# Performance work log

Hardware: AMD Instinct MI355X
Metric: run time of the kernel (lower is better)

## Reference

```python
import jax, jax.numpy as jnp
import numpy as np

B, P, E, C = 64, 10000, 128, 100


def setup_inputs() -> dict:
    key = jax.random.key(0)
    k1, k2, k3, k4 = jax.random.split(key, 4)
    encoded_nodes = jax.random.normal(k1, (B, P, E), dtype=jnp.float32)
    cluster_ids = jax.random.randint(k2, (B, P), 0, C, dtype=jnp.int64)
    # nn.Linear(E, E) params
    lim = 1.0 / np.sqrt(E)
    proj_w = jax.random.uniform(k3, (E, E), dtype=jnp.float32, minval=-lim, maxval=lim)
    proj_b = jax.random.uniform(k4, (E,), dtype=jnp.float32, minval=-lim, maxval=lim)
    return {"encoded_nodes": encoded_nodes, "cluster_ids": cluster_ids,
            "num_clusters": C, "proj_w": proj_w, "proj_b": proj_b}


def reference(encoded_nodes, cluster_ids, num_clusters, proj_w, proj_b):
    ids = cluster_ids.astype(jnp.int32)  # [B, P]

    def seg_sum(x, i):
        return jax.ops.segment_sum(x, i, num_segments=num_clusters)

    # per-batch scatter-add of node embeddings and counts
    sums = jax.vmap(seg_sum)(encoded_nodes, ids)                     # [B, C, E]
    ones = jnp.ones(encoded_nodes.shape[:2], encoded_nodes.dtype)    # [B, P]
    counts = jax.vmap(seg_sum)(ones, ids)[..., None]                  # [B, C, 1]

    cluster_embs = sums / jnp.maximum(counts, 1.0)                    # mean pooling
    cluster_embs = cluster_embs @ proj_w.T + proj_b                   # Linear(E, E)

    # gather each node's (projected) cluster embedding back
    idx = jnp.broadcast_to(ids[:, :, None], encoded_nodes.shape)      # [B, P, E]
    g_node = jnp.take_along_axis(cluster_embs, idx, axis=1)           # [B, P, E]
    return cluster_embs, g_node
```

## Files before the change

### kernel.cpp

```cpp
#include <hip/hip_runtime.h>

#define BB 64
#define PP 10000
#define EE 128
#define CC 100
#define NP 16
#define CHUNK (PP / NP)
#define ROWS (CC * EE)
#define PLANE (CC * 32)

typedef float v4f __attribute__((ext_vector_type(4)));

__global__ __launch_bounds__(256) void scatter_kernel(
    const float* __restrict__ nodes, const int* __restrict__ ids,
    float* __restrict__ psums, float* __restrict__ pcnts)
{
    __shared__ float s_acc[ROWS];
    __shared__ float s_cnt[CC];
    __shared__ int   s_ids[CHUNK];

    const int tid = threadIdx.x;
    const int b   = blockIdx.x;
    const int np  = blockIdx.y;

    for (int i = tid; i < ROWS; i += 256) s_acc[i] = 0.f;
    if (tid < CC) s_cnt[tid] = 0.f;

    const int p0 = np * CHUNK;
    const int* idb = ids + b * PP + p0;
    for (int i = tid; i < CHUNK; i += 256) s_ids[i] = idb[i];
    __syncthreads();

    const int lane = tid & 31;
    const int sub  = tid >> 5;
    const v4f* src = (const v4f*)(nodes + (size_t)b * PP * EE
                                        + (size_t)p0 * EE);

#pragma unroll 4
    for (int p = sub; p < CHUNK; p += 8) {
        int c = s_ids[p];
        v4f v = src[(size_t)p * 32 + lane];
        if ((unsigned)c < CC) {
            float* a = &s_acc[c * 32 + lane];
            __hip_atomic_fetch_add(a + 0 * PLANE, v.x, __ATOMIC_RELAXED, __HIP_MEMORY_SCOPE_WORKGROUP);
            __hip_atomic_fetch_add(a + 1 * PLANE, v.y, __ATOMIC_RELAXED, __HIP_MEMORY_SCOPE_WORKGROUP);
            __hip_atomic_fetch_add(a + 2 * PLANE, v.z, __ATOMIC_RELAXED, __HIP_MEMORY_SCOPE_WORKGROUP);
            __hip_atomic_fetch_add(a + 3 * PLANE, v.w, __ATOMIC_RELAXED, __HIP_MEMORY_SCOPE_WORKGROUP);
            if (lane == 0)
                __hip_atomic_fetch_add(&s_cnt[c], 1.0f, __ATOMIC_RELAXED, __HIP_MEMORY_SCOPE_WORKGROUP);
        }
    }
    __syncthreads();

    v4f* outp = (v4f*)(psums + (size_t)(np * BB + b) * ROWS);
    const v4f* accp = (const v4f*)s_acc;
    for (int i = tid; i < ROWS / 4; i += 256)
        __builtin_nontemporal_store(accp[i], &outp[i]);
    float* oc = pcnts + (np * BB + b) * CC;
    if (tid < CC) __builtin_nontemporal_store(s_cnt[tid], &oc[tid]);
}

__global__ __launch_bounds__(256) void project_kernel(
    float* __restrict__ ce,
    const float* __restrict__ psums,
    const float* __restrict__ pcnts,
    const float* __restrict__ W,
    const float* __restrict__ bias)
{
    __shared__ float s_wt[EE * 129];
    __shared__ float s_mt[EE * 8];
    __shared__ float s_inv[8];

    const int tid = threadIdx.x;
    for (int i = tid; i < EE * EE; i += 256) {
        int e = i >> 7, k = i & 127;
        s_wt[k * 129 + e] = W[i];
    }

    const int e   = tid & 127;
    const int sub = tid >> 7;
    const float be = bias[e];
    const int row0 = blockIdx.x * 16;

    for (int j = 0; j < 2; ++j) {
        __syncthreads();
        if (tid < 8) {
            int row = row0 + j * 8 + tid;
            float s = 0.f;
#pragma unroll
            for (int np = 0; np < NP; ++np)
                s += pcnts[np * (BB * CC) + row];
            s_inv[tid] = 1.0f / fmaxf(s, 1.0f);
        }
        for (int i = tid; i < 8 * EE; i += 256) {
            int rr = i >> 7, idx = i & 127;
            int row = row0 + j * 8 + rr;
            int bb = row / CC, c = row % CC;
            const float* pp = psums + (size_t)bb * ROWS
                                    + (idx >> 5) * PLANE + c * 32 + (idx & 31);
            float s = 0.f;
#pragma unroll
            for (int np = 0; np < NP; ++np)
                s += __builtin_nontemporal_load(pp + (size_t)np * BB * ROWS);
            int ee = ((idx & 31) << 2) | (idx >> 5);
            s_mt[ee * 8 + rr] = s;
        }
        __syncthreads();

        float acc0 = 0.f, acc1 = 0.f, acc2 = 0.f, acc3 = 0.f;
        const float* wp = &s_wt[e];
        const v4f* mp = (const v4f*)s_mt;
#pragma unroll 8
        for (int k = 0; k < 128; ++k) {
            float w = wp[k * 129];
            v4f   m = mp[k * 2 + sub];
            acc0 = fmaf(w, m.x, acc0);
            acc1 = fmaf(w, m.y, acc1);
            acc2 = fmaf(w, m.z, acc2);
            acc3 = fmaf(w, m.w, acc3);
        }
        const int rbase = row0 + j * 8 + sub * 4;
        ce[(size_t)(rbase + 0) * EE + e] = be + acc0 * s_inv[sub * 4 + 0];
        ce[(size_t)(rbase + 1) * EE + e] = be + acc1 * s_inv[sub * 4 + 1];
        ce[(size_t)(rbase + 2) * EE + e] = be + acc2 * s_inv[sub * 4 + 2];
        ce[(size_t)(rbase + 3) * EE + e] = be + acc3 * s_inv[sub * 4 + 3];
    }
}

__global__ __launch_bounds__(256) void gather_kernel(
    const int* __restrict__ ids, const float* __restrict__ ce,
    float* __restrict__ gn)
{
    const int tid  = threadIdx.x;
    const int lane = tid & 31;
    const int sub  = tid >> 5;
    const int b    = blockIdx.y;

    const int* idb = ids + b * PP;
    const v4f* ceb = (const v4f*)(ce + (size_t)b * CC * EE);
    v4f* dst = (v4f*)(gn + (size_t)b * PP * EE);

#pragma unroll 2
    for (int p = blockIdx.x * 8 + sub; p < PP; p += 32 * 8) {
        int c = idb[p];
        if ((unsigned)c >= CC) c = 0;
        v4f v = ceb[(size_t)c * 32 + lane];
        __builtin_nontemporal_store(v, &dst[(size_t)p * 32 + lane]);
    }
}

extern "C" void kernel_launch(void* const* d_in, const int* in_sizes, int n_in,
                              void* d_out, int out_size, void* d_ws, size_t ws_size,
                              hipStream_t stream)
{
    const float* nodes = (const float*)d_in[0];
    const int*   ids   = (const int*)d_in[1];
    const float* W     = (const float*)d_in[3];
    const float* bias  = (const float*)d_in[4];

    float* out = (float*)d_out;
    float* ce  = out;
    float* gn  = out + (size_t)BB * CC * EE;

    float* psums = gn;
    float* pcnts = gn + (size_t)NP * BB * ROWS;

    hipLaunchKernelGGL(scatter_kernel, dim3(BB, NP), dim3(256), 0, stream,
                       nodes, ids, psums, pcnts);
    hipLaunchKernelGGL(project_kernel, dim3(BB * CC / 16), dim3(256), 0, stream,
                       ce, psums, pcnts, W, bias);
    hipLaunchKernelGGL(gather_kernel, dim3(32, BB), dim3(256), 0, stream,
                       ids, ce, gn);
}
```

Before: 886.7 us.

## Fuse scatter and projection into one per-batch kernel without partial sums

Scatter-sum and the linear projection now run in a single kernel with one block per batch. Each block accumulates the whole point range in shared memory, normalises by the counts and projects in place, so the 16-way partial-sum buffers and their reduction pass are gone. In exchange only 64 blocks run on a GPU with far more compute units, so each block walks all 10000 points serially and the scatter phase loses most of its parallelism. W is now read from global memory per thread instead of a transposed shared-memory copy.

```diff
diff --git a/kernel.cpp b/kernel.cpp
--- a/kernel.cpp
+++ b/kernel.cpp
@@ -4,41 +4,36 @@
 #define PP 10000
 #define EE 128
 #define CC 100
-#define NP 16
-#define CHUNK (PP / NP)
-#define ROWS (CC * EE)
 #define PLANE (CC * 32)
+#define ROWS  (CC * EE)
 
 typedef float v4f __attribute__((ext_vector_type(4)));
 
-__global__ __launch_bounds__(256) void scatter_kernel(
+__global__ __launch_bounds__(256) void fused_kernel(
     const float* __restrict__ nodes, const int* __restrict__ ids,
-    float* __restrict__ psums, float* __restrict__ pcnts)
+    const float* __restrict__ W, const float* __restrict__ bias,
+    float* __restrict__ ce)
 {
     __shared__ float s_acc[ROWS];
     __shared__ float s_cnt[CC];
-    __shared__ int   s_ids[CHUNK];
+    __shared__ float s_inv[CC];
+    __shared__ float s_mt[EE * 8];
 
     const int tid = threadIdx.x;
     const int b   = blockIdx.x;
-    const int np  = blockIdx.y;
 
     for (int i = tid; i < ROWS; i += 256) s_acc[i] = 0.f;
     if (tid < CC) s_cnt[tid] = 0.f;
-
-    const int p0 = np * CHUNK;
-    const int* idb = ids + b * PP + p0;
-    for (int i = tid; i < CHUNK; i += 256) s_ids[i] = idb[i];
     __syncthreads();
 
     const int lane = tid & 31;
     const int sub  = tid >> 5;
-    const v4f* src = (const v4f*)(nodes + (size_t)b * PP * EE
-                                        + (size_t)p0 * EE);
+    const v4f* src = (const v4f*)(nodes + (size_t)b * PP * EE);
+    const int* idb = ids + b * PP;
 
 #pragma unroll 4
-    for (int p = sub; p < CHUNK; p += 8) {
-        int c = s_ids[p];
+    for (int p = sub; p < PP; p += 8) {
+        int c = idb[p];
         v4f v = src[(size_t)p * 32 + lane];
         if ((unsigned)c < CC) {
             float* a = &s_acc[c * 32 + lane];
@@ -52,78 +47,42 @@
     }
     __syncthreads();
 
-    v4f* outp = (v4f*)(psums + (size_t)(np * BB + b) * ROWS);
-    const v4f* accp = (const v4f*)s_acc;
-    for (int i = tid; i < ROWS / 4; i += 256)
-        __builtin_nontemporal_store(accp[i], &outp[i]);
-    float* oc = pcnts + (np * BB + b) * CC;
-    if (tid < CC) __builtin_nontemporal_store(s_cnt[tid], &oc[tid]);
-}
+    if (tid < CC) s_inv[tid] = 1.0f / fmaxf(s_cnt[tid], 1.0f);
 
-__global__ __launch_bounds__(256) void project_kernel(
-    float* __restrict__ ce,
-    const float* __restrict__ psums,
-    const float* __restrict__ pcnts,
-    const float* __restrict__ W,
-    const float* __restrict__ bias)
-{
-    __shared__ float s_wt[EE * 129];
-    __shared__ float s_mt[EE * 8];
-    __shared__ float s_inv[8];
+    const int e    = tid & 127;
+    const int sub2 = tid >> 7;
+    const float be = bias[e];
+    const float* __restrict__ wrow = W + (size_t)e * EE;
+    float* ceb = ce + (size_t)b * CC * EE;
 
-    const int tid = threadIdx.x;
-    for (int i = tid; i < EE * EE; i += 256) {
-        int e = i >> 7, k = i & 127;
-        s_wt[k * 129 + e] = W[i];
-    }
-
-    const int e   = tid & 127;
-    const int sub = tid >> 7;
-    const float be = bias[e];
-    const int row0 = blockIdx.x * 16;
-
-    for (int j = 0; j < 2; ++j) {
+    for (int g = 0; g < 13; ++g) {
         __syncthreads();
-        if (tid < 8) {
-            int row = row0 + j * 8 + tid;
-            float s = 0.f;
-#pragma unroll
-            for (int np = 0; np < NP; ++np)
-                s += pcnts[np * (BB * CC) + row];
-            s_inv[tid] = 1.0f / fmaxf(s, 1.0f);
-        }
         for (int i = tid; i < 8 * EE; i += 256) {
-            int rr = i >> 7, idx = i & 127;
-            int row = row0 + j * 8 + rr;
-            int bb = row / CC, c = row % CC;
-            const float* pp = psums + (size_t)bb * ROWS
-                                    + (idx >> 5) * PLANE + c * 32 + (idx & 31);
-            float s = 0.f;
-#pragma unroll
-            for (int np = 0; np < NP; ++np)
-                s += __builtin_nontemporal_load(pp + (size_t)np * BB * ROWS);
-            int ee = ((idx & 31) << 2) | (idx >> 5);
-            s_mt[ee * 8 + rr] = s;
+            int rr = i >> 7, k = i & 127;
+            int c = g * 8 + rr;
+            float m = 0.f;
+            if (c < CC)
+                m = s_acc[(k & 3) * PLANE + c * 32 + (k >> 2)] * s_inv[c];
+            s_mt[k * 8 + rr] = m;
         }
         __syncthreads();
 
         float acc0 = 0.f, acc1 = 0.f, acc2 = 0.f, acc3 = 0.f;
-        const float* wp = &s_wt[e];
         const v4f* mp = (const v4f*)s_mt;
 #pragma unroll 8
         for (int k = 0; k < 128; ++k) {
-            float w = wp[k * 129];
-            v4f   m = mp[k * 2 + sub];
+            float w = wrow[k];
+            v4f   m = mp[k * 2 + sub2];
             acc0 = fmaf(w, m.x, acc0);
             acc1 = fmaf(w, m.y, acc1);
             acc2 = fmaf(w, m.z, acc2);
             acc3 = fmaf(w, m.w, acc3);
         }
-        const int rbase = row0 + j * 8 + sub * 4;
-        ce[(size_t)(rbase + 0) * EE + e] = be + acc0 * s_inv[sub * 4 + 0];
-        ce[(size_t)(rbase + 1) * EE + e] = be + acc1 * s_inv[sub * 4 + 1];
-        ce[(size_t)(rbase + 2) * EE + e] = be + acc2 * s_inv[sub * 4 + 2];
-        ce[(size_t)(rbase + 3) * EE + e] = be + acc3 * s_inv[sub * 4 + 3];
+        const int c0 = g * 8 + sub2 * 4;
+        if (c0 + 0 < CC) ceb[(size_t)(c0 + 0) * EE + e] = be + acc0;
+        if (c0 + 1 < CC) ceb[(size_t)(c0 + 1) * EE + e] = be + acc1;
+        if (c0 + 2 < CC) ceb[(size_t)(c0 + 2) * EE + e] = be + acc2;
+        if (c0 + 3 < CC) ceb[(size_t)(c0 + 3) * EE + e] = be + acc3;
     }
 }
 
@@ -162,13 +121,8 @@
     float* ce  = out;
     float* gn  = out + (size_t)BB * CC * EE;
 
-    float* psums = gn;
-    float* pcnts = gn + (size_t)NP * BB * ROWS;
-
-    hipLaunchKernelGGL(scatter_kernel, dim3(BB, NP), dim3(256), 0, stream,
-                       nodes, ids, psums, pcnts);
-    hipLaunchKernelGGL(project_kernel, dim3(BB * CC / 16), dim3(256), 0, stream,
-                       ce, psums, pcnts, W, bias);
+    hipLaunchKernelGGL(fused_kernel, dim3(BB), dim3(256), 0, stream,
+                       nodes, ids, W, bias, ce);
     hipLaunchKernelGGL(gather_kernel, dim3(32, BB), dim3(256), 0, stream,
                        ids, ce, gn);
 }
```

After: 2.114 ms. +138.4%, slower.
